# Optimization experiments

Measured on AMD Instinct MI355X. Metric: run time of the kernel, lower is better.

The kernel has to match this reference:

```python
import jax, jax.numpy as jnp
import numpy as np

NV = 16384
NF = 32768
B = 4


def _build_laplacian(nv, nf, seed=0):
    # Faithful replication of the torch module's __init__ laplacian construction.
    rng = np.random.RandomState(seed)
    faces = rng.randint(0, nv, size=(nf, 3)).astype(np.int64)
    lap = np.zeros((nv, nv), dtype=np.float32)
    lap[faces[:, 0], faces[:, 1]] = -1
    lap[faces[:, 1], faces[:, 0]] = -1
    lap[faces[:, 1], faces[:, 2]] = -1
    lap[faces[:, 2], faces[:, 1]] = -1
    lap[faces[:, 2], faces[:, 0]] = -1
    lap[faces[:, 0], faces[:, 2]] = -1
    r, c = np.diag_indices(nv)
    lap[r, c] = -lap.sum(1)
    deg = lap[r, c]  # degree per vertex (>= 0)
    # vectorized version of: for i: if lap[i,i] > 0: lap[i,:] /= lap[i,i]
    scale = np.where(deg > 0, 1.0 / np.maximum(deg, 1.0), 1.0).astype(np.float32)
    lap = lap * scale[:, None]
    return lap


def setup_inputs() -> dict:
    key = jax.random.key(0)
    x = jax.random.normal(key, (B, NV, 3), dtype=jnp.float32)
    laplacian = jnp.asarray(_build_laplacian(NV, NF))
    return {"x": x, "laplacian": laplacian}


def reference(x, laplacian):
    # y[b, i, d] = sum_j L[i, j] * x[b, j, d]
    y = jnp.einsum("ij,bjd->bid", laplacian, x)
    # squared L2 norm per batch element (sum over all non-batch dims)
    loss = jnp.sum(y * y, axis=(1, 2))  # [B]
    return loss
```

## Files before the change

kernel.cpp:

```cpp
#include <hip/hip_runtime.h>

#define NV 16384
#define BROWS 16
#define JT 256
#define NT (NV / JT)
#define THREADS 256

typedef const __attribute__((address_space(1))) void* as1_ptr;
typedef __attribute__((address_space(3))) void* as3_ptr;

__device__ __forceinline__ void gload_lds16(const float* g, float* l) {
  __builtin_amdgcn_global_load_lds((as1_ptr)g, (as3_ptr)l, 16, 0, 0);
}

__global__ __launch_bounds__(THREADS, 4) void lap_loss_kernel(
    const float* __restrict__ x, const float* __restrict__ L,
    float* __restrict__ out) {
  __shared__ float lbuf[2][BROWS * JT];

  const int lane = threadIdx.x & 63;
  const int w    = threadIdx.x >> 6;
  const size_t i0 = (size_t)blockIdx.x * BROWS;

  const float* gL[4];
#pragma unroll
  for (int r = 0; r < 4; ++r)
    gL[r] = L + (i0 + 4 * w + r) * NV + lane * 4;

  const float* gx = x + (size_t)w * NV * 3 + lane * 12;

  float acc[BROWS][3];
#pragma unroll
  for (int r = 0; r < BROWS; ++r)
#pragma unroll
    for (int d = 0; d < 3; ++d) acc[r][d] = 0.f;

  float4 xc0 = *(const float4*)(gx + 0);
  float4 xc1 = *(const float4*)(gx + 4);
  float4 xc2 = *(const float4*)(gx + 8);
  asm volatile("" ::: "memory");
#pragma unroll
  for (int r = 0; r < 4; ++r)
    gload_lds16(gL[r], &lbuf[0][(4 * w + r) * JT]);

#pragma unroll 1
  for (int t = 0; t < NT - 1; ++t) {
    const int cur = t & 1;

    const float* gxn = gx + (size_t)(t + 1) * JT * 3;
    float4 xn0 = *(const float4*)(gxn + 0);
    float4 xn1 = *(const float4*)(gxn + 4);
    float4 xn2 = *(const float4*)(gxn + 8);
    asm volatile("" ::: "memory");

#pragma unroll
    for (int r = 0; r < 4; ++r)
      gload_lds16(gL[r] + (size_t)(t + 1) * JT, &lbuf[cur ^ 1][(4 * w + r) * JT]);

    asm volatile("s_waitcnt vmcnt(4)" ::: "memory");
    __builtin_amdgcn_s_barrier();
    asm volatile("" ::: "memory");

    {
      const float xf[12] = {xc0.x, xc0.y, xc0.z, xc0.w,
                            xc1.x, xc1.y, xc1.z, xc1.w,
                            xc2.x, xc2.y, xc2.z, xc2.w};
#pragma unroll
      for (int r = 0; r < BROWS; ++r) {
        float4 lv = *(const float4*)&lbuf[cur][r * JT + lane * 4];
        const float lf[4] = {lv.x, lv.y, lv.z, lv.w};
#pragma unroll
        for (int jj = 0; jj < 4; ++jj)
#pragma unroll
          for (int d = 0; d < 3; ++d)
            acc[r][d] = fmaf(lf[jj], xf[jj * 3 + d], acc[r][d]);
      }
    }

    asm volatile("" ::: "memory");
    __builtin_amdgcn_s_barrier();
    asm volatile("" ::: "memory");

    xc0 = xn0; xc1 = xn1; xc2 = xn2;
  }

  asm volatile("s_waitcnt vmcnt(0)" ::: "memory");
  __builtin_amdgcn_s_barrier();
  asm volatile("" ::: "memory");
  {
    const int cur = (NT - 1) & 1;
    const float xf[12] = {xc0.x, xc0.y, xc0.z, xc0.w,
                          xc1.x, xc1.y, xc1.z, xc1.w,
                          xc2.x, xc2.y, xc2.z, xc2.w};
#pragma unroll
    for (int r = 0; r < BROWS; ++r) {
      float4 lv = *(const float4*)&lbuf[cur][r * JT + lane * 4];
      const float lf[4] = {lv.x, lv.y, lv.z, lv.w};
#pragma unroll
      for (int jj = 0; jj < 4; ++jj)
#pragma unroll
        for (int d = 0; d < 3; ++d)
          acc[r][d] = fmaf(lf[jj], xf[jj * 3 + d], acc[r][d]);
    }
  }

  float s = 0.f;
#pragma unroll
  for (int r = 0; r < BROWS; ++r)
#pragma unroll
    for (int d = 0; d < 3; ++d) {
      float v = acc[r][d];
#pragma unroll
      for (int off = 32; off > 0; off >>= 1)
        v += __shfl_xor(v, off, 64);
      s += v * v;
    }

  if (lane == 0) atomicAdd(&out[w], s);
}

extern "C" void kernel_launch(void* const* d_in, const int* in_sizes, int n_in,
                              void* d_out, int out_size, void* d_ws, size_t ws_size,
                              hipStream_t stream) {
  const float* x = (const float*)d_in[0];
  const float* L = (const float*)d_in[1];
  float* out = (float*)d_out;

  hipMemsetAsync(out, 0, out_size * sizeof(float), stream);

  const int nblocks = NV / BROWS;
  lap_loss_kernel<<<nblocks, THREADS, 0, stream>>>(x, L, out);
}
```

Measured before the change: 240.7 us.

## Deepen L prefetch pipeline to four LDS buffers with three tiles in flight

Replaces the double-buffered global-to-LDS pipeline with a four-buffer ring, prefetching three tiles of the Laplacian ahead, and folds the epilogue tile into the main loop. Per-iteration vmcnt waits are tuned to how many loads are still outstanding. The goal is to hide HBM latency for this bandwidth-bound dense matvec. In exchange, LDS use doubles and the launch bound drops to two blocks per SM, which may reduce occupancy. The hand-counted vmcnt values are brittle if the compiler emits a different number of memory ops.

```diff
diff --git a/kernel.cpp b/kernel.cpp
--- a/kernel.cpp
+++ b/kernel.cpp
@@ -5,6 +5,7 @@
 #define JT 256
 #define NT (NV / JT)
 #define THREADS 256
+#define NBUF 4
 
 typedef const __attribute__((address_space(1))) void* as1_ptr;
 typedef __attribute__((address_space(3))) void* as3_ptr;
@@ -13,10 +14,13 @@
   __builtin_amdgcn_global_load_lds((as1_ptr)g, (as3_ptr)l, 16, 0, 0);
 }
 
-__global__ __launch_bounds__(THREADS, 4) void lap_loss_kernel(
+#define FENCE asm volatile("" ::: "memory")
+#define WAITV(n) asm volatile("s_waitcnt vmcnt(" #n ")" ::: "memory")
+
+__global__ __launch_bounds__(THREADS, 2) void lap_loss_kernel(
     const float* __restrict__ x, const float* __restrict__ L,
     float* __restrict__ out) {
-  __shared__ float lbuf[2][BROWS * JT];
+  __shared__ float lbuf[NBUF][BROWS * JT];
 
   const int lane = threadIdx.x & 63;
   const int w    = threadIdx.x >> 6;
@@ -38,28 +42,41 @@
   float4 xc0 = *(const float4*)(gx + 0);
   float4 xc1 = *(const float4*)(gx + 4);
   float4 xc2 = *(const float4*)(gx + 8);
-  asm volatile("" ::: "memory");
+  FENCE;
 #pragma unroll
-  for (int r = 0; r < 4; ++r)
-    gload_lds16(gL[r], &lbuf[0][(4 * w + r) * JT]);
+  for (int tp = 0; tp < 3; ++tp)
+#pragma unroll
+    for (int r = 0; r < 4; ++r)
+      gload_lds16(gL[r] + (size_t)tp * JT, &lbuf[tp][(4 * w + r) * JT]);
 
 #pragma unroll 1
-  for (int t = 0; t < NT - 1; ++t) {
-    const int cur = t & 1;
+  for (int t = 0; t < NT; ++t) {
+    const int cur = t & (NBUF - 1);
 
-    const float* gxn = gx + (size_t)(t + 1) * JT * 3;
-    float4 xn0 = *(const float4*)(gxn + 0);
-    float4 xn1 = *(const float4*)(gxn + 4);
-    float4 xn2 = *(const float4*)(gxn + 8);
-    asm volatile("" ::: "memory");
+    float4 xn0, xn1, xn2;
+    if (t + 1 < NT) {
+      const float* gxn = gx + (size_t)(t + 1) * JT * 3;
+      xn0 = *(const float4*)(gxn + 0);
+      xn1 = *(const float4*)(gxn + 4);
+      xn2 = *(const float4*)(gxn + 8);
+    }
+    FENCE;
 
+    if (t + 3 < NT) {
 #pragma unroll
-    for (int r = 0; r < 4; ++r)
-      gload_lds16(gL[r] + (size_t)(t + 1) * JT, &lbuf[cur ^ 1][(4 * w + r) * JT]);
+      for (int r = 0; r < 4; ++r)
+        gload_lds16(gL[r] + (size_t)(t + 3) * JT,
+                    &lbuf[(t + 3) & (NBUF - 1)][(4 * w + r) * JT]);
+    }
 
-    asm volatile("s_waitcnt vmcnt(4)" ::: "memory");
+    if (t == 0)            WAITV(15);
+    else if (t == 1)       WAITV(18);
+    else if (t <= NT - 4)  WAITV(21);
+    else if (t == NT - 3)  WAITV(17);
+    else if (t == NT - 2)  WAITV(13);
+    else                   WAITV(0);
     __builtin_amdgcn_s_barrier();
-    asm volatile("" ::: "memory");
+    FENCE;
 
     {
       const float xf[12] = {xc0.x, xc0.y, xc0.z, xc0.w,
@@ -77,31 +94,11 @@
       }
     }
 
-    asm volatile("" ::: "memory");
+    FENCE;
     __builtin_amdgcn_s_barrier();
-    asm volatile("" ::: "memory");
+    FENCE;
 
     xc0 = xn0; xc1 = xn1; xc2 = xn2;
-  }
-
-  asm volatile("s_waitcnt vmcnt(0)" ::: "memory");
-  __builtin_amdgcn_s_barrier();
-  asm volatile("" ::: "memory");
-  {
-    const int cur = (NT - 1) & 1;
-    const float xf[12] = {xc0.x, xc0.y, xc0.z, xc0.w,
-                          xc1.x, xc1.y, xc1.z, xc1.w,
-                          xc2.x, xc2.y, xc2.z, xc2.w};
-#pragma unroll
-    for (int r = 0; r < BROWS; ++r) {
-      float4 lv = *(const float4*)&lbuf[cur][r * JT + lane * 4];
-      const float lf[4] = {lv.x, lv.y, lv.z, lv.w};
-#pragma unroll
-      for (int jj = 0; jj < 4; ++jj)
-#pragma unroll
-        for (int d = 0; d < 3; ++d)
-          acc[r][d] = fmaf(lf[jj], xf[jj * 3 + d], acc[r][d]);
-    }
   }
 
   float s = 0.f;
@@ -117,6 +114,7 @@
     }
 
   if (lane == 0) atomicAdd(&out[w], s);
+
 }
 
 extern "C" void kernel_launch(void* const* d_in, const int* in_sizes, int n_in,
```

Measured after the change: 261.5 us. +8.7%, slower.
